# Kernel optimization log

Hardware: AMD Instinct MI355X
Metric: run time of the kernel (lower is better)

The kernel has to match this reference:

```python
import jax, jax.numpy as jnp
import numpy as np

NUM_HEADS = 4  # init kwarg num_heads


def setup_inputs() -> dict:
    key = jax.random.key(0)
    ks = jax.random.split(key, 9)
    B, N, C, S1 = 8, 2048, 128, 3  # S1 = scale + 1
    w = 1.0 / np.sqrt(C)
    return {
        "pcd": jax.random.normal(ks[0], (B, N, C), jnp.float32),
        "coordinate": jax.random.normal(ks[1], (B, N, 3), jnp.float32),
        "K": 16,
        "Wq": jax.random.normal(ks[2], (C, C), jnp.float32) * w,
        "bq": jax.random.normal(ks[3], (C,), jnp.float32) * w,
        "Wk": jax.random.normal(ks[4], (S1, C, C), jnp.float32) * w,
        "bk": jax.random.normal(ks[5], (S1, C), jnp.float32) * w,
        "Wv": jax.random.normal(ks[6], (C, C), jnp.float32) * w,
        "bv": jax.random.normal(ks[7], (C,), jnp.float32) * w,
    }


def reference(pcd, coordinate, K, Wq, bq, Wk, bk, Wv, bv):
    B, N, C = pcd.shape
    S1 = Wk.shape[0]            # scale + 1
    H = NUM_HEADS
    D = C // H                  # head_dim
    Kt = K * S1                 # one KNN shared by all scales ('OneK')

    # --- KNN in coordinate space (squared euclidean) ---
    sq = jnp.sum(coordinate * coordinate, axis=-1)                      # [B,N]
    dist = sq[:, :, None] + sq[:, None, :] \
        - 2.0 * jnp.einsum('bnc,bmc->bnm', coordinate, coordinate)      # [B,N,N]
    _, idx = jax.lax.top_k(-dist, Kt)                                   # [B,N,Kt]

    # --- gather neighbor features, group_type='diff' (neighbor - center) ---
    nb = jax.vmap(lambda f, i: f[i])(pcd, idx)                          # [B,N,Kt,C]
    diff = nb - pcd[:, :, None, :]                                      # [B,N,Kt,C]

    q = (pcd @ Wq + bq).reshape(B, N, H, D)                             # [B,N,H,D]
    v = (pcd @ Wv + bv).reshape(B, N, H, D)                             # [B,N,H,D]
    inv_sqrt_d = 1.0 / jnp.sqrt(jnp.asarray(D, pcd.dtype))

    # --- per-scale attention maps ('multiple' mode), summed to a per-head gate ---
    attn_map = jnp.zeros((B, N, H), pcd.dtype)
    for i in range(S1):
        feats = diff[:, :, i * K:(i + 1) * K, :]                        # [B,N,K,C]
        k_i = (feats @ Wk[i] + bk[i]).reshape(B, N, K, H, D)            # [B,N,K,H,D]
        logits = jnp.einsum('bnhd,bnkhd->bnhk', q, k_i) * inv_sqrt_d    # [B,N,H,K]
        a = jax.nn.softmax(logits, axis=-1)
        attn_map = attn_map + jnp.sum(a * logits, axis=-1)              # [B,N,H]

    # matmul(attn[...,1,1], value[...,1,D]) -> per-head scalar gate on value
    out = attn_map[..., None] * v                                       # [B,N,H,D]
    return out.reshape(B, N, H * D)
```

## Files before the change

### kernel.cpp

```cpp
#include <hip/hip_runtime.h>
#include <hip/hip_bf16.h>
#include <cstdint>
#include <cstddef>

#define NB_B 8
#define NB_N 2048
#define NB_C 128
#define NB_H 4
#define NB_D 32
#define NB_S1 3
#define NB_K 16
#define NB_KT 48
#define INV_SQRT_D 0.17677669529663688f

#define DPP_F(x, ctrl) \
  __int_as_float(__builtin_amdgcn_update_dpp(0, __float_as_int(x), ctrl, 0xF, 0xF, true))

__device__ __forceinline__ float sum16(float x) {
  x += DPP_F(x, 0xB1);
  x += DPP_F(x, 0x4E);
  x += DPP_F(x, 0x141);
  x += DPP_F(x, 0x140);
  return x;
}
__device__ __forceinline__ float max16(float x) {
  x = fmaxf(x, DPP_F(x, 0xB1));
  x = fmaxf(x, DPP_F(x, 0x4E));
  x = fmaxf(x, DPP_F(x, 0x141));
  x = fmaxf(x, DPP_F(x, 0x140));
  return x;
}

#define DPP_MIN64(g, ctrl)                                                        \
  {                                                                               \
    unsigned int lo_ = (unsigned int)(g), hi_ = (unsigned int)((g) >> 32);        \
    unsigned int l2_ =                                                            \
        (unsigned int)__builtin_amdgcn_update_dpp(0, (int)lo_, ctrl, 0xF, 0xF, true); \
    unsigned int h2_ =                                                            \
        (unsigned int)__builtin_amdgcn_update_dpp(0, (int)hi_, ctrl, 0xF, 0xF, true); \
    unsigned long long o_ = ((unsigned long long)h2_ << 32) | l2_;                \
    if (o_ < (g)) (g) = o_;                                                       \
  }

__device__ __forceinline__ unsigned long long u64min(unsigned long long a,
                                                     unsigned long long b) {
  return a < b ? a : b;
}
__device__ __forceinline__ unsigned long long u64max(unsigned long long a,
                                                     unsigned long long b) {
  return a > b ? a : b;
}

__device__ __forceinline__ void bitonic128(unsigned long long& v0,
                                           unsigned long long& v1, int L) {
#pragma unroll
  for (int k = 2; k <= 128; k <<= 1) {
#pragma unroll
    for (int j = k >> 1; j > 0; j >>= 1) {
      bool up = ((L & (k >> 1)) == 0);
      if (j == 1) {
        unsigned long long lo = u64min(v0, v1), hi = u64max(v0, v1);
        v0 = up ? lo : hi;
        v1 = up ? hi : lo;
      } else {
        int lx = j >> 1;
        unsigned long long o0 = __shfl_xor(v0, lx);
        unsigned long long o1 = __shfl_xor(v1, lx);
        bool keepmin = (((L & lx) == 0) == up);
        v0 = keepmin ? u64min(v0, o0) : u64max(v0, o0);
        v1 = keepmin ? u64min(v1, o1) : u64max(v1, o1);
      }
    }
  }
}

#define BOT2(r0, r1, a0, a1, b0, b1)                          \
  {                                                           \
    r0 = u64min(a0, b0);                                      \
    r1 = u64min(u64max(a0, b0), (a0 < b0) ? (a1) : (b1));     \
  }

__global__ __launch_bounds__(256) void prep_kernel(const float* __restrict__ coord,
                                                   const float* __restrict__ Wk,
                                                   float* __restrict__ sq,
                                                   float* __restrict__ wkT) {
  int tid = blockIdx.x * 256 + threadIdx.x;
  if (tid < NB_B * NB_N) {
    float x = coord[tid * 3 + 0], y = coord[tid * 3 + 1], z = coord[tid * 3 + 2];
    sq[tid] = x * x + y * y + z * z;
  }
  if (tid < NB_S1 * NB_C * NB_C) {
    int i = tid >> 14;
    int rem = tid & 16383;
    int col = rem >> 7, c = rem & 127;
    wkT[tid] = Wk[i * 16384 + c * 128 + col];
  }
}

__global__ __launch_bounds__(256) void topk3_kernel(const float* __restrict__ coord,
                                                    const float* __restrict__ sq,
                                                    int* __restrict__ idx_out) {
  __shared__ unsigned long long srv[4][128];
  const int t = threadIdx.x;
  const int w = t >> 6, l = t & 63;
  const int bn = blockIdx.x * 4 + w;
  const int b = bn >> 11, n = bn & 2047;
  const float* cb = coord + (size_t)b * NB_N * 3;
  const float* sqb = sq + b * NB_N;

  const float cx = cb[n * 3 + 0], cy = cb[n * 3 + 1], cz = cb[n * 3 + 2];
  const float sqn = sqb[n];

  unsigned long long c0[8], c1[8], c2[8], c3[8];
#define DIST_KEY(dst, it)                                                     \
  {                                                                           \
    int m = (it) * 64 + l;                                                    \
    float mx = cb[m * 3 + 0], my = cb[m * 3 + 1], mz = cb[m * 3 + 2];         \
    float d = sqn + sqb[m] - 2.f * (cx * mx + cy * my + cz * mz);             \
    unsigned int db = __float_as_uint(d);                                     \
    unsigned int key = (db & 0x80000000u) ? ~db : (db | 0x80000000u);         \
    dst = ((unsigned long long)key << 32) | (unsigned int)m;                  \
  }
#pragma unroll
  for (int it = 0; it < 8; ++it) DIST_KEY(c0[it], it)
#pragma unroll
  for (int it = 0; it < 8; ++it) DIST_KEY(c1[it], 8 + it)
#pragma unroll
  for (int it = 0; it < 8; ++it) DIST_KEY(c2[it], 16 + it)
#pragma unroll
  for (int it = 0; it < 8; ++it) DIST_KEY(c3[it], 24 + it)
#undef DIST_KEY

#define CE(A, a, b)                                           \
  {                                                           \
    if (A[a] > A[b]) {                                        \
      unsigned long long tmp_ = A[a];                         \
      A[a] = A[b];                                            \
      A[b] = tmp_;                                            \
    }                                                         \
  }
#define SORT8(A)                                              \
  CE(A, 0, 1) CE(A, 2, 3) CE(A, 4, 5) CE(A, 6, 7)             \
  CE(A, 0, 2) CE(A, 1, 3) CE(A, 4, 6) CE(A, 5, 7)             \
  CE(A, 1, 2) CE(A, 5, 6)                                     \
  CE(A, 0, 4) CE(A, 1, 5) CE(A, 2, 6) CE(A, 3, 7)             \
  CE(A, 2, 4) CE(A, 3, 5)                                     \
  CE(A, 1, 2) CE(A, 3, 4) CE(A, 5, 6)
  SORT8(c0) SORT8(c1) SORT8(c2) SORT8(c3)
#undef SORT8
#undef CE

  unsigned long long x0, x1, y0, y1, m1, m2;
  BOT2(x0, x1, c0[0], c0[1], c1[0], c1[1])
  BOT2(y0, y1, c2[0], c2[1], c3[0], c3[1])
  BOT2(m1, m2, x0, x1, y0, y1)

  unsigned long long v0 = m1, v1 = m2;
  bitonic128(v0, v1, l);
  const unsigned long long T = __shfl(v1, 23);

  int cnt = 0;
#pragma unroll
  for (int j = 0; j < 8; ++j) cnt += (c0[j] <= T) ? 1 : 0;
#pragma unroll
  for (int j = 0; j < 8; ++j) cnt += (c1[j] <= T) ? 1 : 0;
#pragma unroll
  for (int j = 0; j < 8; ++j) cnt += (c2[j] <= T) ? 1 : 0;
#pragma unroll
  for (int j = 0; j < 8; ++j) cnt += (c3[j] <= T) ? 1 : 0;
  int inc = cnt;
#pragma unroll
  for (int off = 1; off < 64; off <<= 1) {
    int y = __shfl_up(inc, off);
    if (l >= off) inc += y;
  }
  const int M = __shfl(inc, 63);
  const int excl = inc - cnt;

  if (M <= 128) {
    srv[w][l] = ~0ULL;
    srv[w][l + 64] = ~0ULL;
    int k = excl;
#pragma unroll
    for (int j = 0; j < 8; ++j)
      if (c0[j] <= T) { srv[w][k] = c0[j]; ++k; }
#pragma unroll
    for (int j = 0; j < 8; ++j)
      if (c1[j] <= T) { srv[w][k] = c1[j]; ++k; }
#pragma unroll
    for (int j = 0; j < 8; ++j)
      if (c2[j] <= T) { srv[w][k] = c2[j]; ++k; }
#pragma unroll
    for (int j = 0; j < 8; ++j)
      if (c3[j] <= T) { srv[w][k] = c3[j]; ++k; }
    asm volatile("s_waitcnt lgkmcnt(0)" ::: "memory");
    unsigned long long s0 = srv[w][2 * l];
    unsigned long long s1 = srv[w][2 * l + 1];
    bitonic128(s0, s1, l);
    if (l < 24) {
      int2 o = make_int2((int)(unsigned int)s0, (int)(unsigned int)s1);
      *reinterpret_cast<int2*>(&idx_out[(size_t)bn * NB_KT + 2 * l]) = o;
    }
  } else {
#define POP(A)                                                \
  {                                                           \
    A[0] = A[1]; A[1] = A[2]; A[2] = A[3]; A[3] = A[4];       \
    A[4] = A[5]; A[5] = A[6]; A[6] = A[7]; A[7] = ~0ULL;      \
  }
    unsigned long long lm;
    {
      unsigned long long a = u64min(c0[0], c1[0]);
      unsigned long long b2 = u64min(c2[0], c3[0]);
      lm = u64min(a, b2);
    }
    unsigned int my_out = 0;
    for (int r = 0; r < NB_KT; ++r) {
      unsigned long long g = lm;
      DPP_MIN64(g, 0xB1)
      DPP_MIN64(g, 0x4E)
      DPP_MIN64(g, 0x141)
      DPP_MIN64(g, 0x140)
      {
        unsigned long long o = __shfl_xor(g, 16);
        if (o < g) g = o;
      }
      {
        unsigned long long o = __shfl_xor(g, 32);
        if (o < g) g = o;
      }
      if (l == r) my_out = (unsigned int)g;
      if (lm == g) {
        if (c0[0] == g) { POP(c0) }
        else if (c1[0] == g) { POP(c1) }
        else if (c2[0] == g) { POP(c2) }
        else { POP(c3) }
        unsigned long long a = u64min(c0[0], c1[0]);
        unsigned long long b2 = u64min(c2[0], c3[0]);
        lm = u64min(a, b2);
      }
    }
#undef POP
    if (l < NB_KT) idx_out[(size_t)bn * NB_KT + l] = (int)my_out;
  }
}

__global__ __launch_bounds__(256) void main_kernel(
    const float* __restrict__ pcd,
    const float* __restrict__ Wq, const float* __restrict__ bq,
    const float* __restrict__ bk,
    const float* __restrict__ Wv, const float* __restrict__ bv,
    const float* __restrict__ wkT,
    const int* __restrict__ nbr_idx,
    float* __restrict__ out) {
  __shared__ __align__(16) float self_lds[8][128];
  __shared__ float q_lds[8][132];
  __shared__ float qbk_lds[8][12];

  const int t = threadIdx.x;
  const int w = t >> 6, l = t & 63;
  const int h_l = l >> 4, cg = l & 15;
  const int ws = w * 2;
  const int pt_base = blockIdx.x * 8 + ws;
  const float* pcd_b = pcd + (size_t)((blockIdx.x * 8) >> 11) * NB_N * 128;

#pragma unroll
  for (int p = 0; p < 2; ++p) {
    float2 s = reinterpret_cast<const float2*>(pcd + (size_t)(pt_base + p) * 128)[l];
    reinterpret_cast<float2*>(&self_lds[ws + p][0])[l] = s;
  }

  float qa[2] = {0, 0}, qb[2] = {0, 0};
  float va[2] = {0, 0}, vb[2] = {0, 0};
#pragma unroll 4
  for (int c = 0; c < 128; ++c) {
    float2 wq = reinterpret_cast<const float2*>(Wq + c * 128)[l];
    float2 wv = reinterpret_cast<const float2*>(Wv + c * 128)[l];
#pragma unroll
    for (int p = 0; p < 2; ++p) {
      float x = self_lds[ws + p][c];
      qa[p] = fmaf(wq.x, x, qa[p]); qb[p] = fmaf(wq.y, x, qb[p]);
      va[p] = fmaf(wv.x, x, va[p]); vb[p] = fmaf(wv.y, x, vb[p]);
    }
  }
  {
    float2 bqv = reinterpret_cast<const float2*>(bq)[l];
    float2 bvv = reinterpret_cast<const float2*>(bv)[l];
#pragma unroll
    for (int p = 0; p < 2; ++p) {
      qa[p] += bqv.x; qb[p] += bqv.y; va[p] += bvv.x; vb[p] += bvv.y;
    }
  }
#pragma unroll
  for (int p = 0; p < 2; ++p) {
    q_lds[ws + p][h_l * 33 + 2 * cg] = qa[p];
    q_lds[ws + p][h_l * 33 + 2 * cg + 1] = qb[p];
  }
  if (l < 24) {
    int p = l / 12, g = l % 12;
    int i = g >> 2, h = g & 3;
    const float* qp = &q_lds[ws + p][h * 33];
    const float* bkp = bk + i * 128 + h * 32;
    float s = 0.f;
#pragma unroll 8
    for (int d = 0; d < 32; ++d) s = fmaf(qp[d], bkp[d], s);
    qbk_lds[ws + p][g] = s;
  }

  int nidx[2];
#pragma unroll
  for (int p = 0; p < 2; ++p)
    nidx[p] = (l < 48) ? nbr_idx[(size_t)(pt_base + p) * NB_KT + l] : 0;

  float am[2] = {0, 0};

#pragma unroll
  for (int i = 0; i < 3; ++i) {
    float u[2][8];
#pragma unroll
    for (int p = 0; p < 2; ++p)
#pragma unroll
      for (int k = 0; k < 8; ++k) u[p][k] = 0.f;
    {
      const float* wrow = wkT + i * 16384 + (h_l * 32) * 128 + 4 * cg;
#pragma unroll 4
      for (int d = 0; d < 32; ++d) {
        float4 wa = *reinterpret_cast<const float4*>(wrow + d * 128);
        float4 wb = *reinterpret_cast<const float4*>(wrow + d * 128 + 64);
        float qv[2];
#pragma unroll
        for (int p = 0; p < 2; ++p) qv[p] = q_lds[ws + p][h_l * 33 + d];
#pragma unroll
        for (int p = 0; p < 2; ++p) {
          u[p][0] = fmaf(wa.x, qv[p], u[p][0]);
          u[p][1] = fmaf(wa.y, qv[p], u[p][1]);
          u[p][2] = fmaf(wa.z, qv[p], u[p][2]);
          u[p][3] = fmaf(wa.w, qv[p], u[p][3]);
          u[p][4] = fmaf(wb.x, qv[p], u[p][4]);
          u[p][5] = fmaf(wb.y, qv[p], u[p][5]);
          u[p][6] = fmaf(wb.z, qv[p], u[p][6]);
          u[p][7] = fmaf(wb.w, qv[p], u[p][7]);
        }
      }
    }
    float base[2];
#pragma unroll
    for (int p = 0; p < 2; ++p) {
      const float4* sp = reinterpret_cast<const float4*>(&self_lds[ws + p][4 * cg]);
      float4 sA = sp[0];
      float4 sB = sp[16];
      float sd;
      sd = sA.x * u[p][0];
      sd = fmaf(sA.y, u[p][1], sd);
      sd = fmaf(sA.z, u[p][2], sd);
      sd = fmaf(sA.w, u[p][3], sd);
      sd = fmaf(sB.x, u[p][4], sd);
      sd = fmaf(sB.y, u[p][5], sd);
      sd = fmaf(sB.z, u[p][6], sd);
      sd = fmaf(sB.w, u[p][7], sd);
      sd = sum16(sd);
      base[p] = qbk_lds[ws + p][i * 4 + h_l] - sd;
    }
#pragma unroll
    for (int p = 0; p < 2; ++p) {
      float myl = 0.f;
#pragma unroll
      for (int j = 0; j < 16; ++j) {
        int nb = __builtin_amdgcn_readlane(nidx[p], i * 16 + j);
        const float* rowp = pcd_b + (size_t)(unsigned)nb * 128 + 4 * cg;
        float4 nA = *reinterpret_cast<const float4*>(rowp);
        float4 nB = *reinterpret_cast<const float4*>(rowp + 64);
        float pd;
        pd = nA.x * u[p][0];
        pd = fmaf(nA.y, u[p][1], pd);
        pd = fmaf(nA.z, u[p][2], pd);
        pd = fmaf(nA.w, u[p][3], pd);
        pd = fmaf(nB.x, u[p][4], pd);
        pd = fmaf(nB.y, u[p][5], pd);
        pd = fmaf(nB.z, u[p][6], pd);
        pd = fmaf(nB.w, u[p][7], pd);
        pd = sum16(pd);
        float lg = (pd + base[p]) * INV_SQRT_D;
        if (cg == j) myl = lg;
      }
      float m = max16(myl);
      float e = expf(myl - m);
      float swl = e * myl;
      float se = sum16(e);
      swl = sum16(swl);
      am[p] += swl / se;
    }
  }

#pragma unroll
  for (int p = 0; p < 2; ++p) {
    float2 o = make_float2(am[p] * va[p], am[p] * vb[p]);
    reinterpret_cast<float2*>(out + (size_t)(pt_base + p) * 128)[l] = o;
  }
}

extern "C" void kernel_launch(void* const* d_in, const int* in_sizes, int n_in,
                              void* d_out, int out_size, void* d_ws, size_t ws_size,
                              hipStream_t stream) {
  const float* pcd   = (const float*)d_in[0];
  const float* coord = (const float*)d_in[1];
  const float* Wq = (const float*)d_in[3];
  const float* bq = (const float*)d_in[4];
  const float* Wk = (const float*)d_in[5];
  const float* bk = (const float*)d_in[6];
  const float* Wv = (const float*)d_in[7];
  const float* bv = (const float*)d_in[8];
  float* out = (float*)d_out;

  int*   idx_ws = (int*)d_ws;
  float* sq_ws  = (float*)((char*)d_ws + 3145728);
  float* wkT_ws = (float*)((char*)d_ws + 3211264);

  prep_kernel<<<192, 256, 0, stream>>>(coord, Wk, sq_ws, wkT_ws);
  topk3_kernel<<<NB_B * NB_N / 4, 256, 0, stream>>>(coord, sq_ws, idx_ws);
  main_kernel<<<NB_B * NB_N / 8, 256, 0, stream>>>(pcd, Wq, bq, bk, Wv, bv,
                                                   wkT_ws, idx_ws, out);
}
```

Baseline: 280.8 us.

## Process four points per wave and use butterfly transpose-reduce for neighbor logits

```diff
diff --git a/kernel.cpp b/kernel.cpp
--- a/kernel.cpp
+++ b/kernel.cpp
@@ -15,6 +15,9 @@
 
 #define DPP_F(x, ctrl) \
   __int_as_float(__builtin_amdgcn_update_dpp(0, __float_as_int(x), ctrl, 0xF, 0xF, true))
+
+#define SWZ_F(x, imm) \
+  __int_as_float(__builtin_amdgcn_ds_swizzle(__float_as_int(x), imm))
 
 __device__ __forceinline__ float sum16(float x) {
   x += DPP_F(x, 0xB1);
@@ -244,7 +247,7 @@
   }
 }
 
-__global__ __launch_bounds__(256) void main_kernel(
+__global__ __launch_bounds__(256, 2) void main_kernel(
     const float* __restrict__ pcd,
     const float* __restrict__ Wq, const float* __restrict__ bq,
     const float* __restrict__ bk,
@@ -252,31 +255,31 @@
     const float* __restrict__ wkT,
     const int* __restrict__ nbr_idx,
     float* __restrict__ out) {
-  __shared__ __align__(16) float self_lds[8][128];
-  __shared__ float q_lds[8][132];
-  __shared__ float qbk_lds[8][12];
+  __shared__ __align__(16) float self_lds[16][128];
+  __shared__ float q_lds[16][132];
+  __shared__ float qbk_lds[16][12];
 
   const int t = threadIdx.x;
   const int w = t >> 6, l = t & 63;
   const int h_l = l >> 4, cg = l & 15;
-  const int ws = w * 2;
-  const int pt_base = blockIdx.x * 8 + ws;
-  const float* pcd_b = pcd + (size_t)((blockIdx.x * 8) >> 11) * NB_N * 128;
-
-#pragma unroll
-  for (int p = 0; p < 2; ++p) {
+  const int ws = w * 4;
+  const int pt_base = blockIdx.x * 16 + ws;
+  const float* pcd_b = pcd + (size_t)((blockIdx.x * 16) >> 11) * NB_N * 128;
+
+#pragma unroll
+  for (int p = 0; p < 4; ++p) {
     float2 s = reinterpret_cast<const float2*>(pcd + (size_t)(pt_base + p) * 128)[l];
     reinterpret_cast<float2*>(&self_lds[ws + p][0])[l] = s;
   }
 
-  float qa[2] = {0, 0}, qb[2] = {0, 0};
-  float va[2] = {0, 0}, vb[2] = {0, 0};
-#pragma unroll 4
+  float qa[4] = {0, 0, 0, 0}, qb[4] = {0, 0, 0, 0};
+  float va[4] = {0, 0, 0, 0}, vb[4] = {0, 0, 0, 0};
+#pragma unroll 8
   for (int c = 0; c < 128; ++c) {
     float2 wq = reinterpret_cast<const float2*>(Wq + c * 128)[l];
     float2 wv = reinterpret_cast<const float2*>(Wv + c * 128)[l];
 #pragma unroll
-    for (int p = 0; p < 2; ++p) {
+    for (int p = 0; p < 4; ++p) {
       float x = self_lds[ws + p][c];
       qa[p] = fmaf(wq.x, x, qa[p]); qb[p] = fmaf(wq.y, x, qb[p]);
       va[p] = fmaf(wv.x, x, va[p]); vb[p] = fmaf(wv.y, x, vb[p]);
@@ -286,16 +289,16 @@
     float2 bqv = reinterpret_cast<const float2*>(bq)[l];
     float2 bvv = reinterpret_cast<const float2*>(bv)[l];
 #pragma unroll
-    for (int p = 0; p < 2; ++p) {
+    for (int p = 0; p < 4; ++p) {
       qa[p] += bqv.x; qb[p] += bqv.y; va[p] += bvv.x; vb[p] += bvv.y;
     }
   }
 #pragma unroll
-  for (int p = 0; p < 2; ++p) {
+  for (int p = 0; p < 4; ++p) {
     q_lds[ws + p][h_l * 33 + 2 * cg] = qa[p];
     q_lds[ws + p][h_l * 33 + 2 * cg + 1] = qb[p];
   }
-  if (l < 24) {
+  if (l < 48) {
     int p = l / 12, g = l % 12;
     int i = g >> 2, h = g & 3;
     const float* qp = &q_lds[ws + p][h * 33];
@@ -306,31 +309,31 @@
     qbk_lds[ws + p][g] = s;
   }
 
-  int nidx[2];
-#pragma unroll
-  for (int p = 0; p < 2; ++p)
+  int nidx[4];
+#pragma unroll
+  for (int p = 0; p < 4; ++p)
     nidx[p] = (l < 48) ? nbr_idx[(size_t)(pt_base + p) * NB_KT + l] : 0;
 
-  float am[2] = {0, 0};
+  float am[4] = {0, 0, 0, 0};
 
 #pragma unroll
   for (int i = 0; i < 3; ++i) {
-    float u[2][8];
-#pragma unroll
-    for (int p = 0; p < 2; ++p)
+    float u[4][8];
+#pragma unroll
+    for (int p = 0; p < 4; ++p)
 #pragma unroll
       for (int k = 0; k < 8; ++k) u[p][k] = 0.f;
     {
       const float* wrow = wkT + i * 16384 + (h_l * 32) * 128 + 4 * cg;
-#pragma unroll 4
+#pragma unroll 8
       for (int d = 0; d < 32; ++d) {
         float4 wa = *reinterpret_cast<const float4*>(wrow + d * 128);
         float4 wb = *reinterpret_cast<const float4*>(wrow + d * 128 + 64);
-        float qv[2];
-#pragma unroll
-        for (int p = 0; p < 2; ++p) qv[p] = q_lds[ws + p][h_l * 33 + d];
-#pragma unroll
-        for (int p = 0; p < 2; ++p) {
+        float qv[4];
+#pragma unroll
+        for (int p = 0; p < 4; ++p) qv[p] = q_lds[ws + p][h_l * 33 + d];
+#pragma unroll
+        for (int p = 0; p < 4; ++p) {
           u[p][0] = fmaf(wa.x, qv[p], u[p][0]);
           u[p][1] = fmaf(wa.y, qv[p], u[p][1]);
           u[p][2] = fmaf(wa.z, qv[p], u[p][2]);
@@ -342,9 +345,9 @@
         }
       }
     }
-    float base[2];
-#pragma unroll
-    for (int p = 0; p < 2; ++p) {
+    float base[4];
+#pragma unroll
+    for (int p = 0; p < 4; ++p) {
       const float4* sp = reinterpret_cast<const float4*>(&self_lds[ws + p][4 * cg]);
       float4 sA = sp[0];
       float4 sB = sp[16];
@@ -361,8 +364,8 @@
       base[p] = qbk_lds[ws + p][i * 4 + h_l] - sd;
     }
 #pragma unroll
-    for (int p = 0; p < 2; ++p) {
-      float myl = 0.f;
+    for (int p = 0; p < 4; ++p) {
+      float pp[16];
 #pragma unroll
       for (int j = 0; j < 16; ++j) {
         int nb = __builtin_amdgcn_readlane(nidx[p], i * 16 + j);
@@ -378,10 +381,40 @@
         pd = fmaf(nB.y, u[p][5], pd);
         pd = fmaf(nB.z, u[p][6], pd);
         pd = fmaf(nB.w, u[p][7], pd);
-        pd = sum16(pd);
-        float lg = (pd + base[p]) * INV_SQRT_D;
-        if (cg == j) myl = lg;
-      }
+        pp[j] = pd;
+      }
+      float b8[8];
+#pragma unroll
+      for (int j = 0; j < 8; ++j) {
+        bool hi = (cg & 1) != 0;
+        float mine = hi ? pp[2 * j + 1] : pp[2 * j];
+        float sent = hi ? pp[2 * j] : pp[2 * j + 1];
+        b8[j] = mine + DPP_F(sent, 0xB1);
+      }
+      float b4[4];
+#pragma unroll
+      for (int j = 0; j < 4; ++j) {
+        bool hi = (cg & 2) != 0;
+        float mine = hi ? b8[2 * j + 1] : b8[2 * j];
+        float sent = hi ? b8[2 * j] : b8[2 * j + 1];
+        b4[j] = mine + DPP_F(sent, 0x4E);
+      }
+      float b2[2];
+#pragma unroll
+      for (int j = 0; j < 2; ++j) {
+        bool hi = (cg & 4) != 0;
+        float mine = hi ? b4[2 * j + 1] : b4[2 * j];
+        float sent = hi ? b4[2 * j] : b4[2 * j + 1];
+        b2[j] = mine + SWZ_F(sent, 0x101F);
+      }
+      float b1;
+      {
+        bool hi = (cg & 8) != 0;
+        float mine = hi ? b2[1] : b2[0];
+        float sent = hi ? b2[0] : b2[1];
+        b1 = mine + SWZ_F(sent, 0x201F);
+      }
+      float myl = (b1 + base[p]) * INV_SQRT_D;
       float m = max16(myl);
       float e = expf(myl - m);
       float swl = e * myl;
@@ -392,7 +425,7 @@
   }
 
 #pragma unroll
-  for (int p = 0; p < 2; ++p) {
+  for (int p = 0; p < 4; ++p) {
     float2 o = make_float2(am[p] * va[p], am[p] * vb[p]);
     reinterpret_cast<float2*>(out + (size_t)(pt_base + p) * 128)[l] = o;
   }
@@ -417,6 +450,6 @@
 
   prep_kernel<<<192, 256, 0, stream>>>(coord, Wk, sq_ws, wkT_ws);
   topk3_kernel<<<NB_B * NB_N / 4, 256, 0, stream>>>(coord, sq_ws, idx_ws);
-  main_kernel<<<NB_B * NB_N / 8, 256, 0, stream>>>(pcd, Wq, bq, bk, Wv, bv,
-                                                   wkT_ws, idx_ws, out);
-}
+  main_kernel<<<NB_B * NB_N / 16, 256, 0, stream>>>(pcd, Wq, bq, bk, Wv, bv,
+                                                    wkT_ws, idx_ws, out);
+}
```

Result: no change. 285.6 us (+1.7%).
